# Kernel optimization log

Measured on AMD Instinct MI355X. Metric: run time of the kernel, lower is better.

## Reference

```python
import jax, jax.numpy as jnp
import numpy as np

POOL = 7
NUM_ROIS = 300
H, W, C = 200, 200, 512


def setup_inputs() -> dict:
    key = jax.random.key(0)
    k1, k2, k3, k4, k5 = jax.random.split(key, 5)
    feat = jax.random.normal(k1, (1, H, W, C), dtype=jnp.float32)
    x0 = jax.random.randint(k2, (1, NUM_ROIS), 0, 136)
    y0 = jax.random.randint(k3, (1, NUM_ROIS), 0, 136)
    w = jax.random.randint(k4, (1, NUM_ROIS), 8, 64)
    h = jax.random.randint(k5, (1, NUM_ROIS), 8, 64)
    rois = jnp.stack([x0, y0, w, h], axis=-1).astype(jnp.int32)  # (1, R, 4)
    return {"feat": feat, "rois": rois}


def _pool_one_roi(fmap, roi):
    # fmap: (H, W, C); roi: (4,) int32 = (x0, y0, w, h)
    # Mirrors TF1 bilinear resize (align_corners=False): src = out_idx * in/out.
    x0, y0, w, h = roi[0], roi[1], roi[2], roi[3]
    idx = jnp.arange(POOL, dtype=jnp.float32)
    sy = idx * (h.astype(jnp.float32) / POOL)
    sx = idx * (w.astype(jnp.float32) / POOL)
    y_lo = jnp.floor(sy).astype(jnp.int32)
    x_lo = jnp.floor(sx).astype(jnp.int32)
    y_hi = jnp.minimum(y_lo + 1, h - 1)
    x_hi = jnp.minimum(x_lo + 1, w - 1)
    fy = (sy - y_lo.astype(jnp.float32))[:, None, None]  # (P,1,1)
    fx = (sx - x_lo.astype(jnp.float32))[None, :, None]  # (1,P,1)
    ay_lo, ay_hi = y0 + y_lo, y0 + y_hi
    ax_lo, ax_hi = x0 + x_lo, x0 + x_hi
    v00 = fmap[ay_lo[:, None], ax_lo[None, :]]  # (P,P,C)
    v01 = fmap[ay_lo[:, None], ax_hi[None, :]]
    v10 = fmap[ay_hi[:, None], ax_lo[None, :]]
    v11 = fmap[ay_hi[:, None], ax_hi[None, :]]
    top = v00 * (1.0 - fx) + v01 * fx
    bot = v10 * (1.0 - fx) + v11 * fx
    return top * (1.0 - fy) + bot * fy


def reference(feat, rois):
    # feat: (1,H,W,C), rois: (1,R,4)
    pooled = jax.vmap(_pool_one_roi, in_axes=(None, 0))(feat[0], rois[0])  # (R,P,P,C)
    return pooled[None]  # (1, R, P, P, C)
```

## Files before the change

kernel.cpp:

```cpp
#include <hip/hip_runtime.h>

#define POOL 7
#define NUM_ROIS 300
#define FH 200
#define FW 200
#define FC 512

__global__ __launch_bounds__(128) void roi_pool_kernel(
    const float* __restrict__ feat,
    const int*   __restrict__ rois,
    float*       __restrict__ out)
{
    const int cell = blockIdx.x;
    const int r    = cell / (POOL * POOL);
    const int pp   = cell - r * (POOL * POOL);
    const int py   = pp / POOL;
    const int px   = pp - py * POOL;

    const int x0 = rois[4 * r + 0];
    const int y0 = rois[4 * r + 1];
    const int w  = rois[4 * r + 2];
    const int h  = rois[4 * r + 3];

    const float sy = (float)py * ((float)h / 7.0f);
    const float sx = (float)px * ((float)w / 7.0f);
    const int y_lo = (int)floorf(sy);
    const int x_lo = (int)floorf(sx);
    const int y_hi = min(y_lo + 1, h - 1);
    const int x_hi = min(x_lo + 1, w - 1);
    const float fy = sy - (float)y_lo;
    const float fx = sx - (float)x_lo;

    const float w00 = (1.0f - fy) * (1.0f - fx);
    const float w01 = (1.0f - fy) * fx;
    const float w10 = fy * (1.0f - fx);
    const float w11 = fy * fx;

    const size_t row_lo = (size_t)(y0 + y_lo) * FW;
    const size_t row_hi = (size_t)(y0 + y_hi) * FW;
    const float4* __restrict__ f00 = (const float4*)(feat + (row_lo + (x0 + x_lo)) * FC);
    const float4* __restrict__ f01 = (const float4*)(feat + (row_lo + (x0 + x_hi)) * FC);
    const float4* __restrict__ f10 = (const float4*)(feat + (row_hi + (x0 + x_lo)) * FC);
    const float4* __restrict__ f11 = (const float4*)(feat + (row_hi + (x0 + x_hi)) * FC);
    float4* __restrict__ o = (float4*)(out + (size_t)cell * FC);

    const int t = threadIdx.x;
    const float4 v00 = f00[t];
    const float4 v01 = f01[t];
    const float4 v10 = f10[t];
    const float4 v11 = f11[t];

    float4 res;
    res.x = v00.x * w00 + v01.x * w01 + v10.x * w10 + v11.x * w11;
    res.y = v00.y * w00 + v01.y * w01 + v10.y * w10 + v11.y * w11;
    res.z = v00.z * w00 + v01.z * w01 + v10.z * w10 + v11.z * w11;
    res.w = v00.w * w00 + v01.w * w01 + v10.w * w10 + v11.w * w11;
    o[t] = res;
}

extern "C" void kernel_launch(void* const* d_in, const int* in_sizes, int n_in,
                              void* d_out, int out_size, void* d_ws, size_t ws_size,
                              hipStream_t stream) {
    const float* feat = (const float*)d_in[0];
    const int*   rois = (const int*)d_in[1];
    float*       out  = (float*)d_out;

    const int n_cells = NUM_ROIS * POOL * POOL;
    roi_pool_kernel<<<n_cells, 128, 0, stream>>>(feat, rois, out);
}
```

Measured before the change: 123.5 us.

## Process one pooled row per block and use nontemporal output stores

Each block now handles a whole output row (7 pooled cells) of one ROI instead of a single cell, and loops over px with an unrolled loop. This cuts the block count by a factor of 7 and gives each thread several independent loads in flight, which can raise memory-level parallelism. Output writes use nontemporal stores so the streamed output is less likely to evict reused feature data from cache. The trade-off is fewer blocks in the grid, roughly 2100, which may underfill the GPU.

```diff
diff --git a/kernel.cpp b/kernel.cpp
--- a/kernel.cpp
+++ b/kernel.cpp
@@ -6,56 +6,63 @@
 #define FW 200
 #define FC 512
 
-__global__ __launch_bounds__(128) void roi_pool_kernel(
+typedef float f4 __attribute__((ext_vector_type(4)));
+
+__global__ __launch_bounds__(128) void roi_pool_row_kernel(
     const float* __restrict__ feat,
     const int*   __restrict__ rois,
     float*       __restrict__ out)
 {
-    const int cell = blockIdx.x;
-    const int r    = cell / (POOL * POOL);
-    const int pp   = cell - r * (POOL * POOL);
-    const int py   = pp / POOL;
-    const int px   = pp - py * POOL;
+    const int b  = blockIdx.x;
+    const int r  = b / POOL;
+    const int py = b - r * POOL;
 
     const int x0 = rois[4 * r + 0];
     const int y0 = rois[4 * r + 1];
     const int w  = rois[4 * r + 2];
     const int h  = rois[4 * r + 3];
 
-    const float sy = (float)py * ((float)h / 7.0f);
-    const float sx = (float)px * ((float)w / 7.0f);
-    const int y_lo = (int)floorf(sy);
-    const int x_lo = (int)floorf(sx);
-    const int y_hi = min(y_lo + 1, h - 1);
-    const int x_hi = min(x_lo + 1, w - 1);
-    const float fy = sy - (float)y_lo;
-    const float fx = sx - (float)x_lo;
+    const float hq = (float)h / 7.0f;
+    const float wq = (float)w / 7.0f;
 
-    const float w00 = (1.0f - fy) * (1.0f - fx);
-    const float w01 = (1.0f - fy) * fx;
-    const float w10 = fy * (1.0f - fx);
-    const float w11 = fy * fx;
+    const float sy   = (float)py * hq;
+    const int   y_lo = (int)floorf(sy);
+    const int   y_hi = min(y_lo + 1, h - 1);
+    const float fy   = sy - (float)y_lo;
 
     const size_t row_lo = (size_t)(y0 + y_lo) * FW;
     const size_t row_hi = (size_t)(y0 + y_hi) * FW;
-    const float4* __restrict__ f00 = (const float4*)(feat + (row_lo + (x0 + x_lo)) * FC);
-    const float4* __restrict__ f01 = (const float4*)(feat + (row_lo + (x0 + x_hi)) * FC);
-    const float4* __restrict__ f10 = (const float4*)(feat + (row_hi + (x0 + x_lo)) * FC);
-    const float4* __restrict__ f11 = (const float4*)(feat + (row_hi + (x0 + x_hi)) * FC);
-    float4* __restrict__ o = (float4*)(out + (size_t)cell * FC);
 
     const int t = threadIdx.x;
-    const float4 v00 = f00[t];
-    const float4 v01 = f01[t];
-    const float4 v10 = f10[t];
-    const float4 v11 = f11[t];
+    f4* __restrict__ obase =
+        (f4*)(out + ((size_t)r * (POOL * POOL) + (size_t)py * POOL) * FC);
 
-    float4 res;
-    res.x = v00.x * w00 + v01.x * w01 + v10.x * w10 + v11.x * w11;
-    res.y = v00.y * w00 + v01.y * w01 + v10.y * w10 + v11.y * w11;
-    res.z = v00.z * w00 + v01.z * w01 + v10.z * w10 + v11.z * w11;
-    res.w = v00.w * w00 + v01.w * w01 + v10.w * w10 + v11.w * w11;
-    o[t] = res;
+#pragma unroll
+    for (int px = 0; px < POOL; ++px) {
+        const float sx   = (float)px * wq;
+        const int   x_lo = (int)floorf(sx);
+        const int   x_hi = min(x_lo + 1, w - 1);
+        const float fx   = sx - (float)x_lo;
+
+        const float w00 = (1.0f - fy) * (1.0f - fx);
+        const float w01 = (1.0f - fy) * fx;
+        const float w10 = fy * (1.0f - fx);
+        const float w11 = fy * fx;
+
+        const f4* __restrict__ f00 = (const f4*)(feat + (row_lo + (x0 + x_lo)) * FC);
+        const f4* __restrict__ f01 = (const f4*)(feat + (row_lo + (x0 + x_hi)) * FC);
+        const f4* __restrict__ f10 = (const f4*)(feat + (row_hi + (x0 + x_lo)) * FC);
+        const f4* __restrict__ f11 = (const f4*)(feat + (row_hi + (x0 + x_hi)) * FC);
+
+        const f4 v00 = f00[t];
+        const f4 v01 = f01[t];
+        const f4 v10 = f10[t];
+        const f4 v11 = f11[t];
+
+        const f4 res = v00 * w00 + v01 * w01 + v10 * w10 + v11 * w11;
+
+        __builtin_nontemporal_store(res, &obase[(size_t)px * (FC / 4) + t]);
+    }
 }
 
 extern "C" void kernel_launch(void* const* d_in, const int* in_sizes, int n_in,
@@ -65,6 +72,6 @@
     const int*   rois = (const int*)d_in[1];
     float*       out  = (float*)d_out;
 
-    const int n_cells = NUM_ROIS * POOL * POOL;
-    roi_pool_kernel<<<n_cells, 128, 0, stream>>>(feat, rois, out);
+    const int n_rows = NUM_ROIS * POOL;
+    roi_pool_row_kernel<<<n_rows, 128, 0, stream>>>(feat, rois, out);
 }
```

Result: no change. 125.5 us (+1.6%).
